# Kernel optimization log

Hardware: AMD Instinct MI355X
Metric: run time of the kernel (lower is better)

The kernel has to match this reference:

```python
import jax, jax.numpy as jnp
import numpy as np

B, SV, SQ, D = 32, 4096, 1152, 128
FD = 96  # feature_dim (adaptive pool target and batchnorm channels)
BN_EPS = 1e-5


def setup_inputs() -> dict:
    key = jax.random.key(0)
    k1, k2, k3, k4 = jax.random.split(key, 4)
    return {
        'q': jax.random.normal(k1, (B, SQ, D), dtype=jnp.float32),
        'v': jax.random.normal(k2, (B, SV, D), dtype=jnp.float32),
        'h_mat': jax.random.normal(k3, (1, 3, FD, 1), dtype=jnp.float32),
        'h_bias': jax.random.normal(k4, (1, 3, 1, 1), dtype=jnp.float32),
        'gamma': jnp.ones((FD,), dtype=jnp.float32),
        'beta': jnp.zeros((FD,), dtype=jnp.float32),
    }


def reference(q, v, h_mat, h_bias, gamma, beta):
    b, sv, d = v.shape
    sq = q.shape[1]
    # einsum 'bijk,hcxk,bqiv->bjck' with a=[B,1,Sv,D], h_mat=[1,3,FD,1], b=[B,1,D,Sq]
    # (k broadcasts 1->D, i broadcasts 1->D) factorizes into independent sums:
    sumq = jnp.sum(q, axis=(1, 2))                 # [B] = sum_{i,v} b[b,0,i,v]
    hm = jnp.sum(h_mat, axis=(0, 2, 3))            # [3] = sum_{h,x} h_mat
    # att_maps (post transpose(1,2)): [B,3,Sv,D]
    att = (v[:, None, :, :] * hm[None, :, None, None] * sumq[:, None, None, None]
           + h_bias.reshape(1, 3, 1, 1))
    att = att / jnp.linalg.norm(att, axis=2, keepdims=True)  # L2 norm over Sv
    att = jax.nn.softmax(att, axis=2)                        # softmax over Sv

    # logits = einsum('bikj,bhi,bqvk->bivq', a1, att[:,:,0,:], b1)  -> [B,D,Sq,1]
    att0sum = att[:, :, 0, :].sum(axis=1)          # [B,D] sum over h of att_maps[:,:,0,:]
    qr = q.reshape(b, d, sq)                        # faithful to torch .view memory reshape
    vs = v.sum(axis=1)                              # [B,D] = sum_j a1[b,0,k,j]
    inner = jnp.einsum('bkv,bk->bv', qr, vs)        # [B,Sq]
    logits0 = att0sum[:, :, None] * inner[:, None, :]  # [B,D,Sq]
    # AdaptiveAvgPool1d(FD) on last dim (Sq multiple of FD -> reshape+mean), then transpose
    logits = logits0.reshape(b, d, FD, sq // FD).mean(axis=-1).transpose(0, 2, 1)  # [B,FD,D]

    # loop i=1..h_-1: einsum('bihc,bxv,bqkv->bi') -> per-batch scalar, pooled to [B,FD,1]
    vsum = v.sum(axis=(1, 2))                       # [B]
    qs = qr.sum(axis=2)                             # [B,D] = sum_k b1[b,0,k,v]
    for i in (1, 2):
        attisum = att[:, :, i, :].sum(axis=1)       # [B,D]
        li = vsum * jnp.sum(attisum * qs, axis=1)   # [B]
        logits = logits + li[:, None, None]         # broadcast add of [B,1,1]

    # BatchNorm1d(FD) in training mode: stats over (batch, length) per channel
    mean = logits.mean(axis=(0, 2), keepdims=True)
    var = logits.var(axis=(0, 2), keepdims=True)
    out = (logits - mean) * jax.lax.rsqrt(var + BN_EPS)
    out = out * gamma[None, :, None] + beta[None, :, None]
    return out
```

## Files before the change

### kernel.cpp

```cpp
#include <hip/hip_runtime.h>
#include <math.h>

#define BB 32
#define SV 4096
#define SQ 1152
#define DD 128
#define FD 96
#define NS 32
#define RPC (SV / NS)
#define LOG2E 1.44269504088896340f

#define OFF_G    0
#define OFF_P    393216
#define OFF_ATT0 1179648
#define OFF_LI   1183744
#define OFF_A0   1183776
#define OFF_A0S  1183808
#define OFF_IP   1183840
#define OFF_BNA  1186912
#define OFF_BNB  1187008

__global__ __launch_bounds__(256) void k_pass1(const float* __restrict__ q,
                                               const float* __restrict__ v,
                                               float* __restrict__ ws) {
    __shared__ float red[6][8][DD];
    if (blockIdx.x < 1024) {
        int b = blockIdx.x >> 5, chunk = blockIdx.x & 31;
        int lane = threadIdx.x & 31, rowg = threadIdx.x >> 5;
        int d0 = lane * 4;
        const float* base = v + ((size_t)b * SV + (size_t)chunk * RPC) * DD;
        float s1[4] = {}, s2[4] = {}, s3[4] = {}, s4[4] = {}, s5[4] = {}, s6[4] = {};
        for (int i = 0; i < RPC / 8; i++) {
            float4 x = *reinterpret_cast<const float4*>(base + (size_t)(rowg + 8 * i) * DD + d0);
            float vv[4] = {x.x, x.y, x.z, x.w};
#pragma unroll
            for (int j = 0; j < 4; j++) {
                float a = vv[j], a2 = a * a, a4 = a2 * a2;
                s1[j] += a;       s2[j] += a2;      s3[j] += a2 * a;
                s4[j] += a4;      s5[j] += a4 * a;  s6[j] += a4 * a2;
            }
        }
#pragma unroll
        for (int j = 0; j < 4; j++) {
            red[0][rowg][d0 + j] = s1[j]; red[1][rowg][d0 + j] = s2[j];
            red[2][rowg][d0 + j] = s3[j]; red[3][rowg][d0 + j] = s4[j];
            red[4][rowg][d0 + j] = s5[j]; red[5][rowg][d0 + j] = s6[j];
        }
        __syncthreads();
        for (int t = threadIdx.x; t < 6 * DD; t += 256) {
            int m = t >> 7, d = t & (DD - 1);
            float a = 0;
#pragma unroll
            for (int r = 0; r < 8; r++) a += red[m][r][d];
            ws[OFF_P + ((size_t)(b * NS + chunk) * 6 + m) * DD + d] = a;
        }
    } else {
        int g = (blockIdx.x - 1024) * 256 + threadIdx.x;
        const float4* p = reinterpret_cast<const float4*>(q + (size_t)g * 12);
        float4 a = p[0], b4 = p[1], c = p[2];
        ws[OFF_G + g] = ((a.x + a.y) + (a.z + a.w)) + ((b4.x + b4.y) + (b4.z + b4.w))
                      + ((c.x + c.y) + (c.z + c.w));
    }
}

__global__ __launch_bounds__(256) void k_finalize(const float* __restrict__ v,
                                                  const float* __restrict__ hmat,
                                                  const float* __restrict__ hbias,
                                                  float* __restrict__ ws) {
    int b = blockIdx.x, tid = threadIdx.x;
    __shared__ float Gl[DD * 97];
    __shared__ float qsl[DD], svl[DD];
    __shared__ float hm_l[3], hb_l[3];
    __shared__ float redc[10];
    __shared__ float sumq_sh;
    const float* Gb = ws + OFF_G + (size_t)b * DD * FD;
#pragma unroll
    for (int i = 0; i < 12; i++) {
        int idx = (i * 256 + tid) * 4;
        float4 x = *reinterpret_cast<const float4*>(Gb + idx);
        float xv[4] = {x.x, x.y, x.z, x.w};
#pragma unroll
        for (int j = 0; j < 4; j++) {
            int e = idx + j, dd = e / 96, f = e - dd * 96;
            Gl[dd * 97 + f] = xv[j];
        }
    }
    if (tid >= 128 && tid < 131) {
        int c = tid - 128;
        float h = 0;
        for (int x2 = 0; x2 < FD; x2++) h += hmat[c * FD + x2];
        hm_l[c] = h; hb_l[c] = hbias[c];
    }
    __syncthreads();
    float M1 = 0, M2 = 0, M3 = 0, M4 = 0, M5 = 0, M6 = 0;
    if (tid < 128) {
        const float* P = ws + OFF_P;
#pragma unroll 4
        for (int ch = 0; ch < NS; ch++) {
            const float* p = P + (size_t)(b * NS + ch) * 6 * DD + tid;
            M1 += p[0];      M2 += p[DD];     M3 += p[2 * DD];
            M4 += p[3 * DD]; M5 += p[4 * DD]; M6 += p[5 * DD];
        }
        svl[tid] = M1;
    } else {
        int d = tid - 128;
        float qs = 0;
#pragma unroll 8
        for (int f = 0; f < FD; f++) qs += Gl[d * 97 + f];
        qsl[d] = qs;
    }
    __syncthreads();
    if (tid < 64) {
        float x = qsl[tid] + qsl[tid + 64];
#pragma unroll
        for (int ofs = 32; ofs; ofs >>= 1) x += __shfl_xor(x, ofs, 64);
        if (tid == 0) sumq_sh = x;
    }
    __syncthreads();
    if (tid < 128) {
        float sumq = sumq_sh;
        float v0 = v[((size_t)b * SV + 0) * DD + tid];
        float v1 = v[((size_t)b * SV + 1) * DD + tid];
        float v2 = v[((size_t)b * SV + 2) * DD + tid];
        float att0 = 0, att1 = 0, att2 = 0;
#pragma unroll
        for (int c = 0; c < 3; c++) {
            float alpha = hm_l[c] * sumq, hb = hb_l[c];
            float n2 = alpha * alpha * M2 + 2.f * alpha * hb * M1 + (float)SV * hb * hb;
            float tt = alpha / sqrtf(n2);
            float Z = (float)SV + tt * (M1 + tt * (0.5f * M2 + tt * ((1.f / 6.f) * M3
                    + tt * ((1.f / 24.f) * M4 + tt * ((1.f / 120.f) * M5
                    + tt * (1.f / 720.f) * M6)))));
            float rz = 1.f / Z, tl = tt * LOG2E;
            att0 += exp2f(v0 * tl) * rz;
            att1 += exp2f(v1 * tl) * rz;
            att2 += exp2f(v2 * tl) * rz;
        }
        ws[OFF_ATT0 + b * DD + tid] = att0;
        float qsv = qsl[tid];
        float vals[5] = {att0, att0 * att0, att1 * qsv, att2 * qsv, M1};
#pragma unroll
        for (int i = 0; i < 5; i++) {
            float x = vals[i];
#pragma unroll
            for (int ofs = 32; ofs; ofs >>= 1) x += __shfl_xor(x, ofs, 64);
            if ((tid & 63) == 0) redc[(tid >> 6) * 5 + i] = x;
        }
    }
    __syncthreads();
    if (tid == 0) {
        float a0 = redc[0] + redc[5], a0s = redc[1] + redc[6];
        float r1 = redc[2] + redc[7], r2 = redc[3] + redc[8], vs = redc[4] + redc[9];
        ws[OFF_A0 + b] = a0; ws[OFF_A0S + b] = a0s;
        ws[OFF_LI + b] = vs * (r1 + r2);
    }
    if (tid < FD) {
        float ip = 0;
#pragma unroll 8
        for (int k = 0; k < DD; k++) ip += svl[k] * Gl[k * 97 + tid];
        ws[OFF_IP + b * FD + tid] = ip * (1.0f / 12.0f);
    }
}

__global__ void k_bnstats(const float* __restrict__ gamma, const float* __restrict__ beta,
                          float* __restrict__ ws) {
    const float* ipb = ws + OFF_IP; const float* A0b = ws + OFF_A0;
    const float* A0sb = ws + OFF_A0S; const float* lib = ws + OFF_LI;
    float* bnA = ws + OFF_BNA; float* bnB = ws + OFF_BNB;
    int f = threadIdx.x;
    if (f >= FD) return;
    double Sm = 0, Se2 = 0, Sl = 0;
#pragma unroll 4
    for (int b = 0; b < BB; b++) {
        double ip = ipb[b * FD + f], a0 = A0b[b], a0s = A0sb[b], l = lib[b];
        Sm += ip * a0;
        Se2 += ip * ip * a0s + 2.0 * ip * l * a0 + (double)DD * l * l;
        Sl += l;
    }
    double mean = Sm / ((double)BB * DD) + Sl / (double)BB;
    double var = Se2 / ((double)BB * DD) - mean * mean;
    double rstd = 1.0 / sqrt(var + 1e-5);
    float A = (float)rstd * gamma[f];
    bnA[f] = A; bnB[f] = beta[f] - (float)mean * A;
}

__global__ void k_out(const float* __restrict__ ws, float* __restrict__ out) {
    const float* att0b = ws + OFF_ATT0; const float* ipb = ws + OFF_IP;
    const float* lib = ws + OFF_LI;
    const float* bnA = ws + OFF_BNA; const float* bnB = ws + OFF_BNB;
    int idx = blockIdx.x * blockDim.x + threadIdx.x;
    int k = idx & (DD - 1);
    int bf = idx >> 7;
    int f = bf % FD;
    int b = bf / FD;
    out[idx] = (att0b[b * DD + k] * ipb[b * FD + f] + lib[b]) * bnA[f] + bnB[f];
}

extern "C" void kernel_launch(void* const* d_in, const int* in_sizes, int n_in,
                              void* d_out, int out_size, void* d_ws, size_t ws_size,
                              hipStream_t stream) {
    const float* q     = (const float*)d_in[0];
    const float* v     = (const float*)d_in[1];
    const float* hmat  = (const float*)d_in[2];
    const float* hbias = (const float*)d_in[3];
    const float* gamma = (const float*)d_in[4];
    const float* beta  = (const float*)d_in[5];
    float* out = (float*)d_out;
    float* ws = (float*)d_ws;

    k_pass1<<<2560, 256, 0, stream>>>(q, v, ws);
    k_finalize<<<BB, 256, 0, stream>>>(v, hmat, hbias, ws);
    k_bnstats<<<1, 128, 0, stream>>>(gamma, beta, ws);
    k_out<<<(BB * FD * DD) / 256, 256, 0, stream>>>(ws, out);
}
```

Measured before the change: 126.7 us.

## Fuse pass1, finalize and BN stats into one kernel with last-block atomics

Merges the reduction pass, the per-batch finalize and the batchnorm-stats kernels into a single launch. Per-batch atomic counters let the last arriving block (of 32 v-chunk blocks plus 48 q blocks) do that batch's finalize, and a global counter lets the last finalizing block compute the BN stats. This removes two kernel launches and their serialization gaps. The finalize step now reads G directly from global memory instead of staging it transposed in shared memory, which may give uncoalesced reads in the qs loop, and the extra counters add threadfence overhead.

```diff
diff --git a/kernel.cpp b/kernel.cpp
--- a/kernel.cpp
+++ b/kernel.cpp
@@ -20,14 +20,31 @@
 #define OFF_BNA  1186912
 #define OFF_BNB  1187008
 
-__global__ __launch_bounds__(256) void k_pass1(const float* __restrict__ q,
-                                               const float* __restrict__ v,
-                                               float* __restrict__ ws) {
+__device__ unsigned g_cnt_b[BB];
+__device__ unsigned g_cnt_all;
+
+__global__ __launch_bounds__(256) void k_main(const float* __restrict__ q,
+                                              const float* __restrict__ v,
+                                              const float* __restrict__ hmat,
+                                              const float* __restrict__ hbias,
+                                              const float* __restrict__ gamma,
+                                              const float* __restrict__ beta,
+                                              float* __restrict__ ws) {
     __shared__ float red[6][8][DD];
+    __shared__ float svl[DD], qsl[DD];
+    __shared__ float hm_l[3], hb_l[3];
+    __shared__ float redc[10];
+    __shared__ float sumq_sh;
+    __shared__ unsigned flag_sh, bn_sh;
+
+    const int tid = threadIdx.x;
+    int b_owner;
+
     if (blockIdx.x < 1024) {
-        int b = blockIdx.x >> 5, chunk = blockIdx.x & 31;
-        int lane = threadIdx.x & 31, rowg = threadIdx.x >> 5;
-        int d0 = lane * 4;
+        const int b = blockIdx.x >> 5, chunk = blockIdx.x & 31;
+        b_owner = b;
+        const int lane = tid & 31, rowg = tid >> 5;
+        const int d0 = lane * 4;
         const float* base = v + ((size_t)b * SV + (size_t)chunk * RPC) * DD;
         float s1[4] = {}, s2[4] = {}, s3[4] = {}, s4[4] = {}, s5[4] = {}, s6[4] = {};
         for (int i = 0; i < RPC / 8; i++) {
@@ -47,7 +64,7 @@
             red[4][rowg][d0 + j] = s5[j]; red[5][rowg][d0 + j] = s6[j];
         }
         __syncthreads();
-        for (int t = threadIdx.x; t < 6 * DD; t += 256) {
+        for (int t = tid; t < 6 * DD; t += 256) {
             int m = t >> 7, d = t & (DD - 1);
             float a = 0;
 #pragma unroll
@@ -55,43 +72,28 @@
             ws[OFF_P + ((size_t)(b * NS + chunk) * 6 + m) * DD + d] = a;
         }
     } else {
-        int g = (blockIdx.x - 1024) * 256 + threadIdx.x;
+        int g = (blockIdx.x - 1024) * 256 + tid;
+        b_owner = (blockIdx.x - 1024) / 48;
         const float4* p = reinterpret_cast<const float4*>(q + (size_t)g * 12);
         float4 a = p[0], b4 = p[1], c = p[2];
         ws[OFF_G + g] = ((a.x + a.y) + (a.z + a.w)) + ((b4.x + b4.y) + (b4.z + b4.w))
                       + ((c.x + c.y) + (c.z + c.w));
     }
-}
-
-__global__ __launch_bounds__(256) void k_finalize(const float* __restrict__ v,
-                                                  const float* __restrict__ hmat,
-                                                  const float* __restrict__ hbias,
-                                                  float* __restrict__ ws) {
-    int b = blockIdx.x, tid = threadIdx.x;
-    __shared__ float Gl[DD * 97];
-    __shared__ float qsl[DD], svl[DD];
-    __shared__ float hm_l[3], hb_l[3];
-    __shared__ float redc[10];
-    __shared__ float sumq_sh;
+
+    __syncthreads();
+    if (tid == 0) {
+        __threadfence();
+        unsigned old = atomicAdd(&g_cnt_b[b_owner], 1u);
+        flag_sh = (old == 79u) ? 1u : 0u;
+    }
+    __syncthreads();
+    if (!flag_sh) return;
+
+    __threadfence();
+    if (tid == 0) atomicExch(&g_cnt_b[b_owner], 0u);
+    const int b = b_owner;
     const float* Gb = ws + OFF_G + (size_t)b * DD * FD;
-#pragma unroll
-    for (int i = 0; i < 12; i++) {
-        int idx = (i * 256 + tid) * 4;
-        float4 x = *reinterpret_cast<const float4*>(Gb + idx);
-        float xv[4] = {x.x, x.y, x.z, x.w};
-#pragma unroll
-        for (int j = 0; j < 4; j++) {
-            int e = idx + j, dd = e / 96, f = e - dd * 96;
-            Gl[dd * 97 + f] = xv[j];
-        }
-    }
-    if (tid >= 128 && tid < 131) {
-        int c = tid - 128;
-        float h = 0;
-        for (int x2 = 0; x2 < FD; x2++) h += hmat[c * FD + x2];
-        hm_l[c] = h; hb_l[c] = hbias[c];
-    }
-    __syncthreads();
+
     float M1 = 0, M2 = 0, M3 = 0, M4 = 0, M5 = 0, M6 = 0;
     if (tid < 128) {
         const float* P = ws + OFF_P;
@@ -103,10 +105,19 @@
         }
         svl[tid] = M1;
     } else {
+        if (tid < 131) {
+            int c = tid - 128;
+            float h = 0;
+            for (int x2 = 0; x2 < FD; x2++) h += hmat[c * FD + x2];
+            hm_l[c] = h; hb_l[c] = hbias[c];
+        }
         int d = tid - 128;
         float qs = 0;
-#pragma unroll 8
-        for (int f = 0; f < FD; f++) qs += Gl[d * 97 + f];
+#pragma unroll
+        for (int t4 = 0; t4 < FD / 4; t4++) {
+            float4 x = *reinterpret_cast<const float4*>(Gb + d * FD + t4 * 4);
+            qs += (x.x + x.y) + (x.z + x.w);
+        }
         qsl[d] = qs;
     }
     __syncthreads();
@@ -157,31 +168,39 @@
     if (tid < FD) {
         float ip = 0;
 #pragma unroll 8
-        for (int k = 0; k < DD; k++) ip += svl[k] * Gl[k * 97 + tid];
+        for (int k = 0; k < DD; k++) ip += svl[k] * Gb[k * FD + tid];
         ws[OFF_IP + b * FD + tid] = ip * (1.0f / 12.0f);
     }
-}
-
-__global__ void k_bnstats(const float* __restrict__ gamma, const float* __restrict__ beta,
-                          float* __restrict__ ws) {
-    const float* ipb = ws + OFF_IP; const float* A0b = ws + OFF_A0;
-    const float* A0sb = ws + OFF_A0S; const float* lib = ws + OFF_LI;
-    float* bnA = ws + OFF_BNA; float* bnB = ws + OFF_BNB;
-    int f = threadIdx.x;
-    if (f >= FD) return;
-    double Sm = 0, Se2 = 0, Sl = 0;
+
+    __syncthreads();
+    if (tid == 0) {
+        __threadfence();
+        unsigned old = atomicAdd(&g_cnt_all, 1u);
+        bn_sh = (old == (unsigned)(BB - 1)) ? 1u : 0u;
+    }
+    __syncthreads();
+    if (!bn_sh) return;
+    __threadfence();
+    if (tid == 0) atomicExch(&g_cnt_all, 0u);
+    if (tid < FD) {
+        const float* ipb = ws + OFF_IP;  const float* A0b = ws + OFF_A0;
+        const float* A0sb = ws + OFF_A0S; const float* lib = ws + OFF_LI;
+        const int f = tid;
+        double Sm = 0, Se2 = 0, Sl = 0;
 #pragma unroll 4
-    for (int b = 0; b < BB; b++) {
-        double ip = ipb[b * FD + f], a0 = A0b[b], a0s = A0sb[b], l = lib[b];
-        Sm += ip * a0;
-        Se2 += ip * ip * a0s + 2.0 * ip * l * a0 + (double)DD * l * l;
-        Sl += l;
-    }
-    double mean = Sm / ((double)BB * DD) + Sl / (double)BB;
-    double var = Se2 / ((double)BB * DD) - mean * mean;
-    double rstd = 1.0 / sqrt(var + 1e-5);
-    float A = (float)rstd * gamma[f];
-    bnA[f] = A; bnB[f] = beta[f] - (float)mean * A;
+        for (int bb2 = 0; bb2 < BB; bb2++) {
+            double ip = ipb[bb2 * FD + f], a0 = A0b[bb2], a0s = A0sb[bb2], l = lib[bb2];
+            Sm += ip * a0;
+            Se2 += ip * ip * a0s + 2.0 * ip * l * a0 + (double)DD * l * l;
+            Sl += l;
+        }
+        double mean = Sm / ((double)BB * DD) + Sl / (double)BB;
+        double var = Se2 / ((double)BB * DD) - mean * mean;
+        double rstd = 1.0 / sqrt(var + 1e-5);
+        float A = (float)rstd * gamma[f];
+        (ws + OFF_BNA)[f] = A;
+        (ws + OFF_BNB)[f] = beta[f] - (float)mean * A;
+    }
 }
 
 __global__ void k_out(const float* __restrict__ ws, float* __restrict__ out) {
@@ -208,8 +227,6 @@
     float* out = (float*)d_out;
     float* ws = (float*)d_ws;
 
-    k_pass1<<<2560, 256, 0, stream>>>(q, v, ws);
-    k_finalize<<<BB, 256, 0, stream>>>(v, hmat, hbias, ws);
-    k_bnstats<<<1, 128, 0, stream>>>(gamma, beta, ws);
+    k_main<<<2560, 256, 0, stream>>>(q, v, hmat, hbias, gamma, beta, ws);
     k_out<<<(BB * FD * DD) / 256, 256, 0, stream>>>(ws, out);
 }
```

Result: slower. 242.3 us (+91.3%).

## Fuse finalize, BN stats and output into one kernel with grid barrier

Applied to the files above, without the earlier changes.

Merges the finalize, batchnorm-stats and output kernels into a single 32-block kernel. The blocks synchronize through a software grid barrier built on a global atomic counter, after which each block computes the BN coefficients redundantly and writes its own output slice with float4 stores. This removes two kernel launches and the round-trip of att0 and BN coefficients through global memory. In exchange, the output write is done by only 32 blocks, and the barrier assumes all 32 blocks are co-resident.

```diff
diff --git a/kernel.cpp b/kernel.cpp
--- a/kernel.cpp
+++ b/kernel.cpp
@@ -12,13 +12,12 @@
 
 #define OFF_G    0
 #define OFF_P    393216
-#define OFF_ATT0 1179648
 #define OFF_LI   1183744
 #define OFF_A0   1183776
 #define OFF_A0S  1183808
 #define OFF_IP   1183840
-#define OFF_BNA  1186912
-#define OFF_BNB  1187008
+
+__device__ unsigned g_cnt;
 
 __global__ __launch_bounds__(256) void k_pass1(const float* __restrict__ q,
                                                const float* __restrict__ v,
@@ -63,16 +62,20 @@
     }
 }
 
-__global__ __launch_bounds__(256) void k_finalize(const float* __restrict__ v,
-                                                  const float* __restrict__ hmat,
-                                                  const float* __restrict__ hbias,
-                                                  float* __restrict__ ws) {
+__global__ __launch_bounds__(256) void k_finout(const float* __restrict__ v,
+                                                const float* __restrict__ hmat,
+                                                const float* __restrict__ hbias,
+                                                const float* __restrict__ gamma,
+                                                const float* __restrict__ beta,
+                                                float* __restrict__ ws,
+                                                float* __restrict__ out) {
     int b = blockIdx.x, tid = threadIdx.x;
     __shared__ float Gl[DD * 97];
-    __shared__ float qsl[DD], svl[DD];
+    __shared__ float qsl[DD], svl[DD], att0_sh[DD], ipl[FD];
     __shared__ float hm_l[3], hb_l[3];
     __shared__ float redc[10];
-    __shared__ float sumq_sh;
+    __shared__ float sumq_sh, li_sh;
+    __shared__ float bnA_sh[FD], bnB_sh[FD];
     const float* Gb = ws + OFF_G + (size_t)b * DD * FD;
 #pragma unroll
     for (int i = 0; i < 12; i++) {
@@ -136,7 +139,7 @@
             att1 += exp2f(v1 * tl) * rz;
             att2 += exp2f(v2 * tl) * rz;
         }
-        ws[OFF_ATT0 + b * DD + tid] = att0;
+        att0_sh[tid] = att0;
         float qsv = qsl[tid];
         float vals[5] = {att0, att0 * att0, att1 * qsv, att2 * qsv, M1};
 #pragma unroll
@@ -152,48 +155,64 @@
         float a0 = redc[0] + redc[5], a0s = redc[1] + redc[6];
         float r1 = redc[2] + redc[7], r2 = redc[3] + redc[8], vs = redc[4] + redc[9];
         ws[OFF_A0 + b] = a0; ws[OFF_A0S + b] = a0s;
-        ws[OFF_LI + b] = vs * (r1 + r2);
+        float li = vs * (r1 + r2);
+        ws[OFF_LI + b] = li; li_sh = li;
     }
     if (tid < FD) {
         float ip = 0;
 #pragma unroll 8
         for (int k = 0; k < DD; k++) ip += svl[k] * Gl[k * 97 + tid];
-        ws[OFF_IP + b * FD + tid] = ip * (1.0f / 12.0f);
-    }
-}
-
-__global__ void k_bnstats(const float* __restrict__ gamma, const float* __restrict__ beta,
-                          float* __restrict__ ws) {
-    const float* ipb = ws + OFF_IP; const float* A0b = ws + OFF_A0;
-    const float* A0sb = ws + OFF_A0S; const float* lib = ws + OFF_LI;
-    float* bnA = ws + OFF_BNA; float* bnB = ws + OFF_BNB;
-    int f = threadIdx.x;
-    if (f >= FD) return;
-    double Sm = 0, Se2 = 0, Sl = 0;
+        ip *= (1.0f / 12.0f);
+        ipl[tid] = ip;
+        ws[OFF_IP + b * FD + tid] = ip;
+    }
+
+    __syncthreads();
+    if (tid == 0) {
+        __threadfence();
+        unsigned old = atomicAdd(&g_cnt, 1u);
+        unsigned target = (old / (unsigned)BB + 1u) * (unsigned)BB;
+        while (atomicAdd(&g_cnt, 0u) < target) { __builtin_amdgcn_s_sleep(8); }
+        __threadfence();
+    }
+    __syncthreads();
+
+    if (tid < FD) {
+        const float* ipb = ws + OFF_IP;  const float* A0b = ws + OFF_A0;
+        const float* A0sb = ws + OFF_A0S; const float* lib = ws + OFF_LI;
+        const int f = tid;
+        double Sm = 0, Se2 = 0, Sl = 0;
 #pragma unroll 4
-    for (int b = 0; b < BB; b++) {
-        double ip = ipb[b * FD + f], a0 = A0b[b], a0s = A0sb[b], l = lib[b];
-        Sm += ip * a0;
-        Se2 += ip * ip * a0s + 2.0 * ip * l * a0 + (double)DD * l * l;
-        Sl += l;
-    }
-    double mean = Sm / ((double)BB * DD) + Sl / (double)BB;
-    double var = Se2 / ((double)BB * DD) - mean * mean;
-    double rstd = 1.0 / sqrt(var + 1e-5);
-    float A = (float)rstd * gamma[f];
-    bnA[f] = A; bnB[f] = beta[f] - (float)mean * A;
-}
-
-__global__ void k_out(const float* __restrict__ ws, float* __restrict__ out) {
-    const float* att0b = ws + OFF_ATT0; const float* ipb = ws + OFF_IP;
-    const float* lib = ws + OFF_LI;
-    const float* bnA = ws + OFF_BNA; const float* bnB = ws + OFF_BNB;
-    int idx = blockIdx.x * blockDim.x + threadIdx.x;
-    int k = idx & (DD - 1);
-    int bf = idx >> 7;
-    int f = bf % FD;
-    int b = bf / FD;
-    out[idx] = (att0b[b * DD + k] * ipb[b * FD + f] + lib[b]) * bnA[f] + bnB[f];
+        for (int bb2 = 0; bb2 < BB; bb2++) {
+            double ip = ipb[bb2 * FD + f], a0 = A0b[bb2], a0s = A0sb[bb2], l = lib[bb2];
+            Sm += ip * a0;
+            Se2 += ip * ip * a0s + 2.0 * ip * l * a0 + (double)DD * l * l;
+            Sl += l;
+        }
+        double mean = Sm / ((double)BB * DD) + Sl / (double)BB;
+        double var = Se2 / ((double)BB * DD) - mean * mean;
+        double rstd = 1.0 / sqrt(var + 1e-5);
+        float A = (float)rstd * gamma[f];
+        bnA_sh[f] = A;
+        bnB_sh[f] = beta[f] - (float)mean * A;
+    }
+    __syncthreads();
+
+    float li = li_sh;
+    float* ob = out + (size_t)b * FD * DD;
+#pragma unroll
+    for (int j = 0; j < 12; j++) {
+        int e = j * 256 + tid;
+        int f = e >> 5;
+        int k4 = (e & 31) * 4;
+        float A = bnA_sh[f], Bc = bnB_sh[f], ip = ipl[f];
+        float4 o;
+        o.x = (att0_sh[k4 + 0] * ip + li) * A + Bc;
+        o.y = (att0_sh[k4 + 1] * ip + li) * A + Bc;
+        o.z = (att0_sh[k4 + 2] * ip + li) * A + Bc;
+        o.w = (att0_sh[k4 + 3] * ip + li) * A + Bc;
+        *reinterpret_cast<float4*>(ob + f * DD + k4) = o;
+    }
 }
 
 extern "C" void kernel_launch(void* const* d_in, const int* in_sizes, int n_in,
@@ -209,7 +228,5 @@
     float* ws = (float*)d_ws;
 
     k_pass1<<<2560, 256, 0, stream>>>(q, v, ws);
-    k_finalize<<<BB, 256, 0, stream>>>(v, hmat, hbias, ws);
-    k_bnstats<<<1, 128, 0, stream>>>(gamma, beta, ws);
-    k_out<<<(BB * FD * DD) / 256, 256, 0, stream>>>(ws, out);
+    k_finout<<<BB, 256, 0, stream>>>(v, hmat, hbias, gamma, beta, ws, out);
 }
```

Result: faster. 123.4 us (-2.6%).
